# Optimization experiments

Hardware: AMD Instinct MI355X
Metric: run time of the kernel (lower is better)

## Reference

```python
import jax, jax.numpy as jnp
import numpy as np

EPS = 1e-5

def _conv(x, w, pad):
    return jax.lax.conv_general_dilated(
        x, w, (1, 1), [(pad, pad), (pad, pad)],
        dimension_numbers=('NCHW', 'OIHW', 'NCHW'))

def _bn(x, gamma, beta):
    # BatchNorm2d in training mode: batch statistics over (B,H,W)
    m = jnp.mean(x, axis=(0, 2, 3), keepdims=True)
    v = jnp.var(x, axis=(0, 2, 3), keepdims=True)
    return gamma.reshape(1, -1, 1, 1) * (x - m) * jax.lax.rsqrt(v + EPS) + beta.reshape(1, -1, 1, 1)

def setup_inputs() -> dict:
    key = jax.random.key(0)
    ks = jax.random.split(key, 8)
    B, C, H, W = 2, 128, 128, 128
    E, G, K = 32, 3, 3
    k2 = K * K
    s = 0.05
    return {
        'feat': jax.random.normal(ks[0], (B, C, H, W), jnp.float32),
        'guide': jax.random.normal(ks[1], (B, G, 2 * H, 2 * W), jnp.float32),
        'g_w1': jax.random.normal(ks[2], (E, G, 3, 3), jnp.float32) * s,
        'g_g1': jnp.ones((E,), jnp.float32),
        'g_b1': jnp.zeros((E,), jnp.float32),
        'g_w2': jax.random.normal(ks[3], (E, E, 3, 3), jnp.float32) * s,
        'g_g2': jnp.ones((E,), jnp.float32),
        'g_b2': jnp.zeros((E,), jnp.float32),
        'p_w': jax.random.normal(ks[4], (E, C, 1, 1), jnp.float32) * s,
        'k_w1': jax.random.normal(ks[5], (E, 2 * E, 3, 3), jnp.float32) * s,
        'k_w2': jax.random.normal(ks[6], (k2, E, 1, 1), jnp.float32) * s,
        'k_b2': jnp.zeros((k2,), jnp.float32),
    }

def reference(feat, guide, g_w1, g_g1, g_b1, g_w2, g_g2, g_b2, p_w, k_w1, k_w2, k_b2):
    K = 3
    pad = K // 2
    k2 = K * K
    B, C, H, W = feat.shape
    H2, W2 = 2 * H, 2 * W
    feat_up = jnp.repeat(jnp.repeat(feat, 2, axis=2), 2, axis=3)  # (B,C,H2,W2)
    # guide encoder: conv-BN-ReLU x2
    g = jax.nn.relu(_bn(_conv(guide, g_w1, 1), g_g1, g_b1))
    g = jax.nn.relu(_bn(_conv(g, g_w2, 1), g_g2, g_b2))
    # feature projection: 1x1 conv + ReLU
    f = jax.nn.relu(_conv(feat_up, p_w, 0))
    comb = jnp.concatenate([g, f], axis=1)  # (B,2E,H2,W2)
    kern = _conv(jax.nn.relu(_conv(comb, k_w1, 1)), k_w2, 0) + k_b2.reshape(1, -1, 1, 1)
    kern = jax.nn.softmax(kern, axis=1)  # (B,k2,H2,W2)
    # CARAFE-style reassembly without materializing the unfold tensor:
    # out[b,c,y,x] = sum_{dy,dx} kern[b,dy*K+dx,y,x] * feat_up_pad[b,c,y+dy,x+dx]
    fp = jnp.pad(feat_up, ((0, 0), (0, 0), (pad, pad), (pad, pad)))
    out = jnp.zeros((B, C, H2, W2), feat.dtype)
    for i in range(k2):  # fixed small k2=9 taps
        dy, dx = i // K, i % K
        out = out + kern[:, i:i + 1] * fp[:, :, dy:dy + H2, dx:dx + W2]
    return out
```

## Files before the change

kernel.cpp:

```cpp
#include <hip/hip_runtime.h>
#include <hip/hip_bf16.h>

#define EPS 1e-5f


typedef unsigned short ushort_t;
typedef __attribute__((ext_vector_type(8))) short short8v;
typedef __attribute__((ext_vector_type(4))) float f32x4;

__device__ __forceinline__ int swz(int b) { return b ^ (((b >> 7) & 7) << 4); }
__device__ __forceinline__ float bf2f(ushort_t u) {
    unsigned int t = ((unsigned int)u) << 16;
    return __builtin_bit_cast(float, t);
}
__device__ __forceinline__ ushort_t f2bf(float f) {
    __hip_bfloat16 h = (__hip_bfloat16)f;
    return __builtin_bit_cast(ushort_t, h);
}

__device__ __forceinline__ void ab_inline(
    const float* __restrict__ part, const float* __restrict__ gamma,
    const float* __restrict__ beta, float* red, int tid)
{
    int col = tid & 63, quart = tid >> 6;
    float s = 0.f;
    const float* p = part + (size_t)(quart * 64) * 64 + col;
#pragma unroll 8
    for (int bq = 0; bq < 64; ++bq) s += p[(size_t)bq * 64];
    red[quart * 64 + col] = s;
    __syncthreads();
    if (tid < 64)
        red[256 + tid] = red[tid] + red[64 + tid] + red[128 + tid] + red[192 + tid];
    __syncthreads();
    if (tid < 32) {
        float S  = red[256 + (tid >> 1) * 4 + (tid & 1) * 2];
        float SS = red[256 + (tid >> 1) * 4 + (tid & 1) * 2 + 1];
        const float n = 131072.f;
        float mean = S / n;
        float var = SS / n - mean * mean;
        float a = gamma[tid] * rsqrtf(var + EPS);
        red[320 + tid] = a;
        red[352 + tid] = beta[tid] - mean * a;
    }
    __syncthreads();
}

__global__ __launch_bounds__(256) void k_phase1(
    const float* __restrict__ guide, const float* __restrict__ w1,
    const float* __restrict__ w2, const float* __restrict__ kw1,
    const float* __restrict__ pw, const float* __restrict__ feat,
    ushort_t* __restrict__ x1, ushort_t* __restrict__ fs,
    ushort_t* __restrict__ wpk)
{
    __shared__ __align__(16) char lds[40960];
    int tid = threadIdx.x;
    int blk = blockIdx.x;

    if (blk < 512) {
        float* smu = (float*)lds;
        int b = blk >> 8;
        int tile = blk & 255;
        int ty0 = (tile >> 4) << 4, tx0 = (tile & 15) << 4;

        for (int i = tid; i < 972; i += 256) {
            int c = i / 324;
            int rem = i - c * 324;
            int r = rem / 18, cl = rem - r * 18;
            int yy = ty0 + r - 1, xx = tx0 + cl - 1;
            float v = 0.f;
            if (yy >= 0 && yy < 256 && xx >= 0 && xx < 256)
                v = guide[((b * 3 + c) * 256 + yy) * 256 + xx];
            smu[c * 342 + r * 19 + cl] = v;
        }
        __syncthreads();

        int r = tid >> 4, cl = tid & 15;
        float t[27];
#pragma unroll
        for (int c = 0; c < 3; ++c)
#pragma unroll
            for (int ky = 0; ky < 3; ++ky)
#pragma unroll
                for (int kx = 0; kx < 3; ++kx)
                    t[c * 9 + ky * 3 + kx] = smu[c * 342 + (r + ky) * 19 + cl + kx];
        int y = ty0 + r, x = tx0 + cl;
        ushort_t pk[32];
#pragma unroll 4
        for (int e = 0; e < 32; ++e) {
            float acc = 0.f;
#pragma unroll
            for (int k = 0; k < 27; ++k)
                acc += t[k] * w1[e * 27 + k];
            pk[e] = f2bf(acc);
        }
        ushort_t* dst = x1 + ((size_t)(b * 65536 + y * 256 + x)) * 32;
#pragma unroll
        for (int h = 0; h < 4; ++h)
            *(uint4*)(dst + h * 8) = *(uint4*)(pk + h * 8);
    } else if (blk < 768) {
        int row = blk - 512;
        int b = row >> 7, yl = row & 127;
        ushort_t* pwl = (ushort_t*)(lds + 32768);

        for (int i = tid; i < 4096; i += 256) {
            int j = i & 7, l = (i >> 3) & 63, nt = (i >> 9) & 1, ks = i >> 10;
            int e = nt * 16 + (l & 15);
            int c = ks * 32 + (l >> 4) * 8 + j;
            pwl[i] = f2bf(pw[e * 128 + c]);
        }
        int x = tid & 127, cg = tid >> 7;
        const float* fb = feat + ((size_t)b << 21) + yl * 128 + x;
#pragma unroll
        for (int p = 0; p < 8; ++p) {
            int c0 = p * 16 + cg * 8;
            ushort_t pk[8];
#pragma unroll
            for (int j = 0; j < 8; ++j)
                pk[j] = f2bf(fb[(size_t)(c0 + j) << 14]);
            *(uint4*)(lds + swz(x * 256 + c0 * 2)) = *(uint4*)pk;
        }
        __syncthreads();

        int w = tid >> 6, l = tid & 63, lm = l & 15, lg = l >> 4;
        int px0 = w * 32;
        f32x4 acc[2][2] = {};
        const short8v* gB = (const short8v*)pwl;
#pragma unroll
        for (int ks = 0; ks < 4; ++ks) {
            short8v B0 = gB[(ks * 2 + 0) * 64 + l];
            short8v B1 = gB[(ks * 2 + 1) * 64 + l];
#pragma unroll
            for (int m = 0; m < 2; ++m) {
                short8v A = *(const short8v*)(
                    lds + swz((px0 + m * 16 + lm) * 256 + ks * 64 + lg * 16));
                acc[m][0] = __builtin_amdgcn_mfma_f32_16x16x32_bf16(A, B0, acc[m][0], 0, 0, 0);
                acc[m][1] = __builtin_amdgcn_mfma_f32_16x16x32_bf16(A, B1, acc[m][1], 0, 0, 0);
            }
        }
        __syncthreads();
#pragma unroll
        for (int m = 0; m < 2; ++m)
#pragma unroll
            for (int nt = 0; nt < 2; ++nt)
#pragma unroll
                for (int rg = 0; rg < 4; ++rg) {
                    int px = px0 + m * 16 + lg * 4 + rg;
                    int e = nt * 16 + lm;
                    *(ushort_t*)(lds + swz(px * 64 + e * 2)) =
                        f2bf(fmaxf(acc[m][nt][rg], 0.f));
                }
        __syncthreads();
        if (tid < 128) {
            ushort_t* dst = fs + ((size_t)(b * 16384 + yl * 128 + tid)) * 32;
#pragma unroll
            for (int h = 0; h < 4; ++h)
                *(uint4*)(dst + h * 8) = *(uint4*)(lds + swz(tid * 64 + h * 16));
        }
    } else {
        int i = (blk - 768) * 256 + tid;
        if (i < 9216) {
            int j = i & 7, l = (i >> 3) & 63, nt = (i >> 9) & 1, t = i >> 10;
            int e = nt * 16 + (l & 15);
            int k = (l >> 4) * 8 + j;
            wpk[i] = f2bf(w2[(e * 32 + k) * 9 + t]);
        } else {
            int i2 = i - 9216;
            int j = i2 & 7, l = (i2 >> 3) & 63, nt = (i2 >> 9) & 1;
            int kk = (i2 >> 10) & 1, t = i2 >> 11;
            int e = nt * 16 + (l & 15);
            int k = kk * 32 + (l >> 4) * 8 + j;
            wpk[i] = f2bf(kw1[(e * 64 + k) * 9 + t]);
        }
    }
}

__global__ __launch_bounds__(256) void k_statsP(
    const ushort_t* __restrict__ x, float* __restrict__ part)
{
    int tid = threadIdx.x, bk = blockIdx.x;
    int p = tid >> 4, c2 = tid & 15;
    float s0 = 0.f, ss0 = 0.f, s1 = 0.f, ss1 = 0.f;
    const ushort_t* base = x + ((size_t)bk * 512) * 32 + c2 * 2;
    for (int i = 0; i < 32; ++i) {
        unsigned int v = *(const unsigned int*)(base + (size_t)(i * 16 + p) * 32);
        float a = bf2f((ushort_t)(v & 0xffff));
        float c = bf2f((ushort_t)(v >> 16));
        s0 += a; ss0 += a * a; s1 += c; ss1 += c * c;
    }
    __shared__ float red[256][4];
    red[tid][0] = s0; red[tid][1] = ss0; red[tid][2] = s1; red[tid][3] = ss1;
    __syncthreads();
    if (tid < 64) {
        int c2s = tid & 15, vs = tid >> 4;
        float t = 0.f;
        for (int pp = 0; pp < 16; ++pp) t += red[pp * 16 + c2s][vs];
        part[bk * 64 + c2s * 4 + vs] = t;
    }
}

__global__ __launch_bounds__(256) void k_conv2(
    const ushort_t* __restrict__ x1, const float* __restrict__ part,
    const float* __restrict__ gamma, const float* __restrict__ beta,
    const ushort_t* __restrict__ w2pk, ushort_t* __restrict__ x2)
{
    __shared__ __align__(16) char lds[22272];
    float* red = (float*)(lds + 20736);
    int tid = threadIdx.x;
    ab_inline(part, gamma, beta, red, tid);
    const float* ab1 = red + 320;

    int b = blockIdx.x >> 8, tile = blockIdx.x & 255;
    int ty0 = (tile >> 4) << 4, tx0 = (tile & 15) << 4;

    for (int i = tid; i < 1296; i += 256) {
        int px = i >> 2, c8 = i & 3;
        int r = px / 18, cl = px - r * 18;
        int yy = ty0 + r - 1, xx = tx0 + cl - 1;
        ushort_t pk[8];
        if (yy >= 0 && yy < 256 && xx >= 0 && xx < 256) {
            const ushort_t* src = x1 + ((size_t)(b * 65536 + yy * 256 + xx)) * 32 + c8 * 8;
            uint4 raw = *(const uint4*)src;
            const ushort_t* rs = (const ushort_t*)&raw;
#pragma unroll
            for (int j = 0; j < 8; ++j) {
                int c = c8 * 8 + j;
                pk[j] = f2bf(fmaxf(ab1[c] * bf2f(rs[j]) + ab1[32 + c], 0.f));
            }
        } else {
#pragma unroll
            for (int j = 0; j < 8; ++j) pk[j] = 0;
        }
        *(uint4*)(lds + swz(px * 64 + c8 * 16)) = *(uint4*)pk;
    }
    __syncthreads();

    int w = tid >> 6, l = tid & 63, lm = l & 15, lg = l >> 4;
    f32x4 acc[4][2] = {};
    const short8v* gB = (const short8v*)w2pk;
#pragma unroll
    for (int t = 0; t < 9; ++t) {
        int ky = t / 3, kx = t % 3;
        short8v B0 = gB[(t * 2 + 0) * 64 + l];
        short8v B1 = gB[(t * 2 + 1) * 64 + l];
#pragma unroll
        for (int m = 0; m < 4; ++m) {
            int px = (w * 4 + m + ky) * 18 + lm + kx;
            short8v A = *(const short8v*)(lds + swz(px * 64 + lg * 16));
            acc[m][0] = __builtin_amdgcn_mfma_f32_16x16x32_bf16(A, B0, acc[m][0], 0, 0, 0);
            acc[m][1] = __builtin_amdgcn_mfma_f32_16x16x32_bf16(A, B1, acc[m][1], 0, 0, 0);
        }
    }
    __syncthreads();
#pragma unroll
    for (int m = 0; m < 4; ++m)
#pragma unroll
        for (int nt = 0; nt < 2; ++nt)
#pragma unroll
            for (int rg = 0; rg < 4; ++rg) {
                int px = (w * 4 + m) * 16 + lg * 4 + rg;
                int e = nt * 16 + lm;
                *(ushort_t*)(lds + swz(px * 64 + e * 2)) = f2bf(acc[m][nt][rg]);
            }
    __syncthreads();
    {
        int px = tid, r = px >> 4, cl = px & 15;
        int yy = ty0 + r, xx = tx0 + cl;
        ushort_t* dst = x2 + ((size_t)(b * 65536 + yy * 256 + xx)) * 32;
#pragma unroll
        for (int h = 0; h < 4; ++h)
            *(uint4*)(dst + h * 8) = *(uint4*)(lds + swz(px * 64 + h * 16));
    }
}

__global__ __launch_bounds__(256) void k_tail(
    const ushort_t* __restrict__ x2, const float* __restrict__ part,
    const float* __restrict__ gamma, const float* __restrict__ beta,
    const ushort_t* __restrict__ fs, const ushort_t* __restrict__ kw1pk,
    const float* __restrict__ kw2, const float* __restrict__ kb2,
    const float* __restrict__ feat, float* __restrict__ out)
{
    __shared__ __align__(16) char lds[38784];
    int tid = threadIdx.x;

    int p = blockIdx.x;
    int xcd = p & 7, q = p >> 3;
    int g = xcd * 64 + (q >> 1);
    int b = g >> 8;
    int rem = g & 255;
    int ty0 = (rem >> 3) << 3;
    int tx0 = (((rem & 7) << 1) | (q & 1)) << 4;

    float* redz = (float*)(lds + 32640);
    ab_inline(part, gamma, beta, redz, tid);
    const float* ab2 = redz + 320;

    for (int i = tid; i < 1440; i += 256) {
        int px = i >> 3, c8 = i & 7;
        int r = px / 18, cl = px - r * 18;
        int yy = ty0 + r - 1, xx = tx0 + cl - 1;
        ushort_t pk[8];
        if (yy >= 0 && yy < 256 && xx >= 0 && xx < 256) {
            if (c8 < 4) {
                const ushort_t* src = x2 + ((size_t)(b * 65536 + yy * 256 + xx)) * 32 + c8 * 8;
                uint4 raw = *(const uint4*)src;
                const ushort_t* rs = (const ushort_t*)&raw;
#pragma unroll
                for (int j = 0; j < 8; ++j) {
                    int c = c8 * 8 + j;
                    pk[j] = f2bf(fmaxf(ab2[c] * bf2f(rs[j]) + ab2[32 + c], 0.f));
                }
            } else {
                const ushort_t* src = fs + ((size_t)(b * 16384 + (yy >> 1) * 128 + (xx >> 1))) * 32 + (c8 - 4) * 8;
                *(uint4*)pk = *(const uint4*)src;
            }
        } else {
#pragma unroll
            for (int j = 0; j < 8; ++j) pk[j] = 0;
        }
        *(uint4*)(lds + swz(px * 128 + c8 * 16)) = *(uint4*)pk;
    }
    __syncthreads();

    int w = tid >> 6, l = tid & 63, lm = l & 15, lg = l >> 4;
    f32x4 acc[2][2] = {};
    {
        const short8v* gB = (const short8v*)kw1pk;
#pragma unroll
        for (int t = 0; t < 9; ++t) {
            int ky = t / 3, kx = t % 3;
#pragma unroll
            for (int kk = 0; kk < 2; ++kk) {
                short8v B0 = gB[(t * 4 + kk * 2 + 0) * 64 + l];
                short8v B1 = gB[(t * 4 + kk * 2 + 1) * 64 + l];
#pragma unroll
                for (int m = 0; m < 2; ++m) {
                    int mt = w * 2 + m;
                    int px = (mt + ky) * 18 + lm + kx;
                    short8v A = *(const short8v*)(lds + swz(px * 128 + kk * 64 + lg * 16));
                    acc[m][0] = __builtin_amdgcn_mfma_f32_16x16x32_bf16(A, B0, acc[m][0], 0, 0, 0);
                    acc[m][1] = __builtin_amdgcn_mfma_f32_16x16x32_bf16(A, B1, acc[m][1], 0, 0, 0);
                }
            }
        }
    }
    __syncthreads();
#pragma unroll
    for (int m = 0; m < 2; ++m)
#pragma unroll
        for (int nt = 0; nt < 2; ++nt)
#pragma unroll
            for (int rg = 0; rg < 4; ++rg) {
                int px = (w * 2 + m) * 16 + lg * 4 + rg;
                int e = nt * 16 + lm;
                *(float*)(lds + swz(px * 128 + e * 4)) = acc[m][nt][rg];
            }
    __syncthreads();

    float* zbuf = (float*)(lds + 32640);
    if (tid < 128) {
        int px = tid;
        float v[32];
#pragma unroll
        for (int h = 0; h < 8; ++h) {
            float4 qd = *(const float4*)(lds + swz(px * 128 + h * 16));
            v[h * 4 + 0] = qd.x; v[h * 4 + 1] = qd.y; v[h * 4 + 2] = qd.z; v[h * 4 + 3] = qd.w;
        }
        float z[9];
#pragma unroll
        for (int i = 0; i < 9; ++i) z[i] = kb2[i];
#pragma unroll
        for (int e = 0; e < 32; ++e) {
            float ae = fmaxf(v[e], 0.f);
#pragma unroll
            for (int i = 0; i < 9; ++i)
                z[i] += ae * kw2[i * 32 + e];
        }
        float m = z[0];
#pragma unroll
        for (int i = 1; i < 9; ++i) m = fmaxf(m, z[i]);
        float sum = 0.f;
#pragma unroll
        for (int i = 0; i < 9; ++i) { z[i] = expf(z[i] - m); sum += z[i]; }
        float inv = 1.f / sum;
#pragma unroll
        for (int i = 0; i < 9; ++i) zbuf[px * 12 + i] = z[i] * inv;
    }
    __syncthreads();

    float* lf2 = (float*)lds;
    {
        int ty0l = ty0 >> 1, tx0l = tx0 >> 1;
        for (int i = tid; i < 3072; i += 256) {
            int c = i / 24;
            int rem2 = i - c * 24;
            int rt = rem2 >> 2, qq = rem2 & 3;
            int ylo = ty0l + rt - 1;
            int cb = tx0l - 4 + qq * 4;
            float4 v = { 0.f, 0.f, 0.f, 0.f };
            if (ylo >= 0 && ylo < 128 && cb >= 0 && cb < 125)
                v = *(const float4*)(feat + (((size_t)(b * 128 + c)) << 14) + ylo * 128 + cb);
            const float* vp = (const float*)&v;
#pragma unroll
            for (int j = 0; j < 4; ++j) {
                int k = cb + j - (tx0l - 1);
                if (k >= 0 && k < 10)
                    lf2[(rt * 10 + k) * 136 + c] = vp[j];
            }
        }
    }
    __syncthreads();

    {
        int px = tid & 127, chalf = tid >> 7;
        int r = px >> 4, cl = px & 15;
        int y = ty0 + r, x = tx0 + cl;
        int ry = r & 1, rx = cl & 1;
        float z[9];
#pragma unroll
        for (int i = 0; i < 9; ++i) z[i] = zbuf[px * 12 + i];
        float zr[2][3];
#pragma unroll
        for (int dx = 0; dx < 3; ++dx) {
            if (ry == 0) { zr[0][dx] = z[dx];             zr[1][dx] = z[3 + dx] + z[6 + dx]; }
            else         { zr[0][dx] = z[dx] + z[3 + dx]; zr[1][dx] = z[6 + dx]; }
        }
        float co00, co01, co10, co11;
        if (rx == 0) { co00 = zr[0][0];            co01 = zr[0][1] + zr[0][2];
                       co10 = zr[1][0];            co11 = zr[1][1] + zr[1][2]; }
        else         { co00 = zr[0][0] + zr[0][1]; co01 = zr[0][2];
                       co10 = zr[1][0] + zr[1][1]; co11 = zr[1][2]; }
        int py0 = (r >> 1) + ry, px0c = (cl >> 1) + rx;
        int p00 = py0 * 10 + px0c;
        float* op = out + (((size_t)b * 128) * 256 + y) * 256 + x;
#pragma unroll 4
        for (int gg = 0; gg < 16; ++gg) {
            int c4 = chalf * 16 + gg;
            float4 f00 = *(const float4*)(lf2 + p00 * 136 + c4 * 4);
            float4 f01 = *(const float4*)(lf2 + (p00 + 1) * 136 + c4 * 4);
            float4 f10 = *(const float4*)(lf2 + (p00 + 10) * 136 + c4 * 4);
            float4 f11 = *(const float4*)(lf2 + (p00 + 11) * 136 + c4 * 4);
            const float* a00 = (const float*)&f00;
            const float* a01 = (const float*)&f01;
            const float* a10 = (const float*)&f10;
            const float* a11 = (const float*)&f11;
#pragma unroll
            for (int j = 0; j < 4; ++j) {
                float o = co00 * a00[j] + co01 * a01[j]
                        + co10 * a10[j] + co11 * a11[j];
                op[(size_t)(c4 * 4 + j) * 65536] = o;
            }
        }
    }
}

extern "C" void kernel_launch(void* const* d_in, const int* in_sizes, int n_in,
                              void* d_out, int out_size, void* d_ws, size_t ws_size,
                              hipStream_t stream)
{
    const float* feat  = (const float*)d_in[0];
    const float* guide = (const float*)d_in[1];
    const float* g_w1  = (const float*)d_in[2];
    const float* g_g1  = (const float*)d_in[3];
    const float* g_b1  = (const float*)d_in[4];
    const float* g_w2  = (const float*)d_in[5];
    const float* g_g2  = (const float*)d_in[6];
    const float* g_b2  = (const float*)d_in[7];
    const float* p_w   = (const float*)d_in[8];
    const float* k_w1  = (const float*)d_in[9];
    const float* k_w2  = (const float*)d_in[10];
    const float* k_b2  = (const float*)d_in[11];

    float* out = (float*)d_out;

    ushort_t* x1 = (ushort_t*)out;
    ushort_t* x2 = (ushort_t*)(out + 2097152);

    ushort_t* fs    = (ushort_t*)d_ws;
    ushort_t* wpk   = (ushort_t*)((char*)d_ws + 2097152);
    float*    partA = (float*)((char*)d_ws + 2152448);
    float*    partB = (float*)((char*)d_ws + 2217984);
    ushort_t* w2pk  = wpk;
    ushort_t* kw1pk = wpk + 9216;

    k_phase1<<<876, 256, 0, stream>>>(guide, g_w1, g_w2, k_w1, p_w, feat,
                                      x1, fs, wpk);
    k_statsP<<<256, 256, 0, stream>>>(x1, partA);
    k_conv2<<<512, 256, 0, stream>>>(x1, partA, g_g1, g_b1, w2pk, x2);
    k_statsP<<<256, 256, 0, stream>>>(x2, partB);
    k_tail<<<1024, 256, 0, stream>>>(x2, partB, g_g2, g_b2, fs, kw1pk,
                                     k_w2, k_b2, feat, out);
}
```

Measured before the change: 72.28 us.

## Fuse BatchNorm statistics partial sums into conv producer kernels

Removes the two standalone k_statsP launches and computes per-tile channel sum and sum-of-squares inside k_phase1 and k_conv2, using values already held in LDS. Each producer block writes 64 partials, so the consumer reduction now sums 512 partial rows instead of 256. This saves two kernel launches and a full re-read of x1 and x2 from global memory. In exchange it adds extra LDS traffic and barriers in the producers, and doubles the partial-reduction work done in every consumer block.

```diff
diff --git a/kernel.cpp b/kernel.cpp
--- a/kernel.cpp
+++ b/kernel.cpp
@@ -24,9 +24,9 @@
 {
     int col = tid & 63, quart = tid >> 6;
     float s = 0.f;
-    const float* p = part + (size_t)(quart * 64) * 64 + col;
+    const float* p = part + (size_t)(quart * 128) * 64 + col;
 #pragma unroll 8
-    for (int bq = 0; bq < 64; ++bq) s += p[(size_t)bq * 64];
+    for (int bq = 0; bq < 128; ++bq) s += p[(size_t)bq * 64];
     red[quart * 64 + col] = s;
     __syncthreads();
     if (tid < 64)
@@ -50,7 +50,7 @@
     const float* __restrict__ w2, const float* __restrict__ kw1,
     const float* __restrict__ pw, const float* __restrict__ feat,
     ushort_t* __restrict__ x1, ushort_t* __restrict__ fs,
-    ushort_t* __restrict__ wpk)
+    ushort_t* __restrict__ wpk, float* __restrict__ part1)
 {
     __shared__ __align__(16) char lds[40960];
     int tid = threadIdx.x;
@@ -84,6 +84,7 @@
                 for (int kx = 0; kx < 3; ++kx)
                     t[c * 9 + ky * 3 + kx] = smu[c * 342 + (r + ky) * 19 + cl + kx];
         int y = ty0 + r, x = tx0 + cl;
+        float* sdump = (float*)(lds + 4224);
         ushort_t pk[32];
 #pragma unroll 4
         for (int e = 0; e < 32; ++e) {
@@ -92,11 +93,36 @@
             for (int k = 0; k < 27; ++k)
                 acc += t[k] * w1[e * 27 + k];
             pk[e] = f2bf(acc);
+            sdump[tid * 33 + e] = bf2f(pk[e]);
         }
         ushort_t* dst = x1 + ((size_t)(b * 65536 + y * 256 + x)) * 32;
 #pragma unroll
         for (int h = 0; h < 4; ++h)
             *(uint4*)(dst + h * 8) = *(uint4*)(pk + h * 8);
+
+        __syncthreads();
+        {
+            int ch = tid & 31, seg = tid >> 5;
+            float s = 0.f, q = 0.f;
+#pragma unroll 8
+            for (int i = 0; i < 32; ++i) {
+                float v = sdump[(seg * 32 + i) * 33 + ch];
+                s += v; q += v * v;
+            }
+            float* segbuf = (float*)(lds + 38016);
+            segbuf[(seg * 32 + ch) * 2 + 0] = s;
+            segbuf[(seg * 32 + ch) * 2 + 1] = q;
+            __syncthreads();
+            if (tid < 64) {
+                int c = tid >> 1, isq = tid & 1;
+                float tt = 0.f;
+#pragma unroll
+                for (int g = 0; g < 8; ++g)
+                    tt += segbuf[(g * 32 + c) * 2 + isq];
+                int col = (c >> 1) * 4 + (c & 1) * 2 + isq;
+                part1[(size_t)blk * 64 + col] = tt;
+            }
+        }
     } else if (blk < 768) {
         int row = blk - 512;
         int b = row >> 7, yl = row & 127;
@@ -174,39 +200,16 @@
     }
 }
 
-__global__ __launch_bounds__(256) void k_statsP(
-    const ushort_t* __restrict__ x, float* __restrict__ part)
+__global__ __launch_bounds__(256) void k_conv2(
+    const ushort_t* __restrict__ x1, const float* __restrict__ part1,
+    const float* __restrict__ gamma, const float* __restrict__ beta,
+    const ushort_t* __restrict__ w2pk, ushort_t* __restrict__ x2,
+    float* __restrict__ part2)
 {
-    int tid = threadIdx.x, bk = blockIdx.x;
-    int p = tid >> 4, c2 = tid & 15;
-    float s0 = 0.f, ss0 = 0.f, s1 = 0.f, ss1 = 0.f;
-    const ushort_t* base = x + ((size_t)bk * 512) * 32 + c2 * 2;
-    for (int i = 0; i < 32; ++i) {
-        unsigned int v = *(const unsigned int*)(base + (size_t)(i * 16 + p) * 32);
-        float a = bf2f((ushort_t)(v & 0xffff));
-        float c = bf2f((ushort_t)(v >> 16));
-        s0 += a; ss0 += a * a; s1 += c; ss1 += c * c;
-    }
-    __shared__ float red[256][4];
-    red[tid][0] = s0; red[tid][1] = ss0; red[tid][2] = s1; red[tid][3] = ss1;
-    __syncthreads();
-    if (tid < 64) {
-        int c2s = tid & 15, vs = tid >> 4;
-        float t = 0.f;
-        for (int pp = 0; pp < 16; ++pp) t += red[pp * 16 + c2s][vs];
-        part[bk * 64 + c2s * 4 + vs] = t;
-    }
-}
-
-__global__ __launch_bounds__(256) void k_conv2(
-    const ushort_t* __restrict__ x1, const float* __restrict__ part,
-    const float* __restrict__ gamma, const float* __restrict__ beta,
-    const ushort_t* __restrict__ w2pk, ushort_t* __restrict__ x2)
-{
-    __shared__ __align__(16) char lds[22272];
+    __shared__ __align__(16) char lds[22784];
     float* red = (float*)(lds + 20736);
     int tid = threadIdx.x;
-    ab_inline(part, gamma, beta, red, tid);
+    ab_inline(part1, gamma, beta, red, tid);
     const float* ab1 = red + 320;
 
     int b = blockIdx.x >> 8, tile = blockIdx.x & 255;
@@ -270,10 +273,35 @@
         for (int h = 0; h < 4; ++h)
             *(uint4*)(dst + h * 8) = *(uint4*)(lds + swz(px * 64 + h * 16));
     }
+
+    {
+        int ch = tid & 31, seg = tid >> 5;
+        float s = 0.f, q = 0.f;
+#pragma unroll 8
+        for (int i = 0; i < 32; ++i) {
+            int px = seg * 32 + i;
+            float v = bf2f(*(const ushort_t*)(lds + swz(px * 64 + ch * 2)));
+            s += v; q += v * v;
+        }
+        float* segbuf = (float*)(lds + 20736);
+        __syncthreads();
+        segbuf[(seg * 32 + ch) * 2 + 0] = s;
+        segbuf[(seg * 32 + ch) * 2 + 1] = q;
+        __syncthreads();
+        if (tid < 64) {
+            int c = tid >> 1, isq = tid & 1;
+            float tt = 0.f;
+#pragma unroll
+            for (int g = 0; g < 8; ++g)
+                tt += segbuf[(g * 32 + c) * 2 + isq];
+            int col = (c >> 1) * 4 + (c & 1) * 2 + isq;
+            part2[(size_t)blockIdx.x * 64 + col] = tt;
+        }
+    }
 }
 
 __global__ __launch_bounds__(256) void k_tail(
-    const ushort_t* __restrict__ x2, const float* __restrict__ part,
+    const ushort_t* __restrict__ x2, const float* __restrict__ part2,
     const float* __restrict__ gamma, const float* __restrict__ beta,
     const ushort_t* __restrict__ fs, const ushort_t* __restrict__ kw1pk,
     const float* __restrict__ kw2, const float* __restrict__ kb2,
@@ -291,7 +319,7 @@
     int tx0 = (((rem & 7) << 1) | (q & 1)) << 4;
 
     float* redz = (float*)(lds + 32640);
-    ab_inline(part, gamma, beta, redz, tid);
+    ab_inline(part2, gamma, beta, redz, tid);
     const float* ab2 = redz + 320;
 
     for (int i = tid; i < 1440; i += 256) {
@@ -478,15 +506,13 @@
     ushort_t* fs    = (ushort_t*)d_ws;
     ushort_t* wpk   = (ushort_t*)((char*)d_ws + 2097152);
     float*    partA = (float*)((char*)d_ws + 2152448);
-    float*    partB = (float*)((char*)d_ws + 2217984);
+    float*    partB = (float*)((char*)d_ws + 2283520);
     ushort_t* w2pk  = wpk;
     ushort_t* kw1pk = wpk + 9216;
 
     k_phase1<<<876, 256, 0, stream>>>(guide, g_w1, g_w2, k_w1, p_w, feat,
-                                      x1, fs, wpk);
-    k_statsP<<<256, 256, 0, stream>>>(x1, partA);
-    k_conv2<<<512, 256, 0, stream>>>(x1, partA, g_g1, g_b1, w2pk, x2);
-    k_statsP<<<256, 256, 0, stream>>>(x2, partB);
+                                      x1, fs, wpk, partA);
+    k_conv2<<<512, 256, 0, stream>>>(x1, partA, g_g1, g_b1, w2pk, x2, partB);
     k_tail<<<1024, 256, 0, stream>>>(x2, partB, g_g2, g_b2, fs, kw1pk,
                                      k_w2, k_b2, feat, out);
 }
```

Measured after the change: 71.47 us (median of 2 runs). No clear change (-1.1%).
